# Performance work log

Measured on AMD Instinct MI355X. Metric: run time of the kernel, lower is better.

Reference implementation:

```python
import jax, jax.numpy as jnp
import numpy as np

B, V, E, H, L = 1024, 50257, 512, 512, 2


def setup_inputs() -> dict:
    key = jax.random.key(0)
    ks = jax.random.split(key, 12)
    s = 1.0 / np.sqrt(H)
    inp = {
        "x": jax.random.randint(ks[0], (B,), 0, V),
        "hidden": jnp.zeros((2 * L, B, H), jnp.float32),
        "embed": jax.random.normal(ks[1], (V, E), jnp.float32) * 0.02,
        # layer 0: input size E; layer 1: input size 2H (bidirectional concat)
        "Wih0": jax.random.uniform(ks[2], (2, 3 * H, E), jnp.float32, -s, s),
        "Whh0": jax.random.uniform(ks[3], (2, 3 * H, H), jnp.float32, -s, s),
        "bih0": jax.random.uniform(ks[4], (2, 3 * H), jnp.float32, -s, s),
        "bhh0": jax.random.uniform(ks[5], (2, 3 * H), jnp.float32, -s, s),
        "Wih1": jax.random.uniform(ks[6], (2, 3 * H, 2 * H), jnp.float32, -s, s),
        "Whh1": jax.random.uniform(ks[7], (2, 3 * H, H), jnp.float32, -s, s),
        "bih1": jax.random.uniform(ks[8], (2, 3 * H), jnp.float32, -s, s),
        "bhh1": jax.random.uniform(ks[9], (2, 3 * H), jnp.float32, -s, s),
        "Wproj": jax.random.uniform(ks[10], (V, E), jnp.float32, -1.0 / np.sqrt(E), 1.0 / np.sqrt(E)),
        "bproj": jax.random.uniform(ks[11], (V,), jnp.float32, -1.0 / np.sqrt(E), 1.0 / np.sqrt(E)),
    }
    return inp


def _gru_cell(x, h, Wih, Whh, bih, bhh):
    # PyTorch GRU cell: gates ordered (r, z, n)
    gi = x @ Wih.T + bih            # [B, 3H]
    gh = h @ Whh.T + bhh            # [B, 3H]
    ir, iz, inn = jnp.split(gi, 3, axis=-1)
    hr, hz, hn = jnp.split(gh, 3, axis=-1)
    r = jax.nn.sigmoid(ir + hr)
    z = jax.nn.sigmoid(iz + hz)
    n = jnp.tanh(inn + r * hn)
    return (1.0 - z) * n + z * h


def reference(x, hidden, embed, Wih0, Whh0, bih0, bhh0, Wih1, Whh1, bih1, bhh1, Wproj, bproj):
    inp = embed[x]                  # [B, E] embedding lookup; seq_len == 1
    layer_params = [(Wih0, Whh0, bih0, bhh0), (Wih1, Whh1, bih1, bhh1)]
    new_h = []
    for l, (Wih, Whh, bih, bhh) in enumerate(layer_params):
        # single timestep: fwd and bwd directions each do one cell step on the same input
        hf = _gru_cell(inp, hidden[2 * l],     Wih[0], Whh[0], bih[0], bhh[0])
        hb = _gru_cell(inp, hidden[2 * l + 1], Wih[1], Whh[1], bih[1], bhh[1])
        new_h += [hf, hb]
        inp = jnp.concatenate([hf, hb], axis=-1)   # [B, 2H]
    # x[:, :, hidden_dim:] -> backward-direction output of top layer, then transpose(0,1)
    out = hb[:, None, :]                            # [B, 1, H]
    logits = out @ Wproj.T + bproj                  # [B, 1, V]
    probs = jax.nn.softmax(logits, axis=-1)
    return probs, jnp.stack(new_h, axis=0)          # ([B,1,V], [2L, B, H])
```

## Files before the change

### kernel.cpp

```cpp
#include <hip/hip_runtime.h>


#define Bsz 1024
#define Hs  512
#define Vv  50257
#define VP2 50432
#define NG  1536
#define NPB2 197
#define NPBF 393

typedef __bf16 bf16x8 __attribute__((ext_vector_type(8)));
typedef float  floatx4 __attribute__((ext_vector_type(4)));

__device__ __forceinline__ unsigned short f2bf(float f) {
  unsigned int u = __builtin_bit_cast(unsigned int, f);
  u += 0x7fffu + ((u >> 16) & 1u);
  return (unsigned short)(u >> 16);
}

__device__ __forceinline__ float bf2f(unsigned short u) {
  unsigned int x = (unsigned int)u << 16;
  return __builtin_bit_cast(float, x);
}

__device__ __forceinline__ void cvt4(const float* src, unsigned short* dst) {
  float4 f = *(const float4*)src;
  unsigned int lo = (unsigned int)f2bf(f.x) | ((unsigned int)f2bf(f.y) << 16);
  unsigned int hi = (unsigned int)f2bf(f.z) | ((unsigned int)f2bf(f.w) << 16);
  *(uint2*)dst = make_uint2(lo, hi);
}

__device__ __forceinline__ void g2lds16(const void* g, void* l) {
  unsigned long long gv = (unsigned long long)g;
  unsigned int lv = (unsigned int)(unsigned long long)l;
  __builtin_amdgcn_global_load_lds(
      (const __attribute__((address_space(1))) unsigned int*)gv,
      (__attribute__((address_space(3))) unsigned int*)lv,
      16, 0, 0);
}

__device__ __forceinline__ void stage_half512(const unsigned short* src, long long rowBase,
                                              unsigned short* tile, int half, int kOff,
                                              int w, int l) {
#pragma unroll
  for (int i = 0; i < 2; ++i) {
    int t16 = (i * 8 + w) * 64 + l;
    int row = t16 >> 3, c = t16 & 7;
    int sc = c ^ (row & 7);
    const unsigned short* g = src + (rowBase + half * 128 + row) * 512ll + kOff + sc * 8;
    g2lds16(g, (char*)tile + half * 16384 + (i * 8 + w) * 1024 + l * 16);
  }
}

#define PHASEQ(Q)                                                                           \
  do {                                                                                      \
    bf16x8 afr[2][2];                                                                       \
    _Pragma("unroll") for (int mm = 0; mm < 2; ++mm)                                        \
    _Pragma("unroll") for (int ks = 0; ks < 2; ++ks) {                                      \
      int rowA = wr * 128 + (2 * (Q) + mm) * 16 + r16;                                      \
      int slot = (ks * 4 + g) ^ (rowA & 7);                                                 \
      afr[mm][ks] = *(const bf16x8*)((const char*)Ac + rowA * 128 + slot * 16);             \
    }                                                                                       \
    __builtin_amdgcn_s_barrier();                                                           \
    __builtin_amdgcn_s_setprio(1);                                                          \
    _Pragma("unroll") for (int ks = 0; ks < 2; ++ks)                                        \
    _Pragma("unroll") for (int mm = 0; mm < 2; ++mm)                                        \
    _Pragma("unroll") for (int nf = 0; nf < 4; ++nf)                                        \
      acc[2 * (Q) + mm][nf] = __builtin_amdgcn_mfma_f32_16x16x32_bf16(                      \
          afr[mm][ks], bfr[nf][ks], acc[2 * (Q) + mm][nf], 0, 0, 0);                        \
    __builtin_amdgcn_s_setprio(0);                                                          \
    __builtin_amdgcn_s_barrier();                                                           \
  } while (0)

__global__ __launch_bounds__(512, 2) void gemm_proj8(const unsigned short* A, const unsigned short* Bw,
                                                     const float* biasp, unsigned short* stash,
                                                     float* partial) {
  __shared__ alignas(16) unsigned short Ab[2][16384];
  __shared__ alignas(16) unsigned short Bb[2][16384];
  __shared__ float rowpart[256][4];
  const int tid = threadIdx.x;
  const int w = tid >> 6, l = tid & 63;
  const int wr = w >> 2, wc = w & 3;
  const int g = l >> 4, r16 = l & 15;
  int orig = blockIdx.x;
  int xcd = orig & 7, slot = orig >> 3;
  int wgid = (xcd < 4 ? xcd * 99 : 396 + (xcd - 4) * 98) + slot;
  int mt = wgid & 3, nt = wgid >> 2;

  floatx4 acc[8][4];
  floatx4 zero = {0.f, 0.f, 0.f, 0.f};
#pragma unroll
  for (int i = 0; i < 8; ++i)
#pragma unroll
    for (int j = 0; j < 4; ++j) acc[i][j] = zero;

  const long long mrb = (long long)mt * 256;
  const long long nrb = (long long)nt * 256;

  stage_half512(Bw, nrb, Bb[0], 0, 0, w, l);
  stage_half512(Bw, nrb, Bb[0], 1, 0, w, l);
  stage_half512(A,  mrb, Ab[0], 0, 0, w, l);
  stage_half512(A,  mrb, Ab[0], 1, 0, w, l);
  stage_half512(Bw, nrb, Bb[1], 0, 64, w, l);
  stage_half512(Bw, nrb, Bb[1], 1, 64, w, l);
  asm volatile("s_waitcnt vmcnt(4)" ::: "memory");
  __builtin_amdgcn_s_barrier();

#pragma unroll
  for (int t = 0; t < 8; ++t) {
    const int c = t & 1;
    const unsigned short* Ac = Ab[c];
    const unsigned short* Bc = Bb[c];
    if (t > 0) {
      if (t < 7) asm volatile("s_waitcnt vmcnt(4)" ::: "memory");
      else       asm volatile("s_waitcnt vmcnt(0)" ::: "memory");
      __builtin_amdgcn_s_barrier();
    }
    if (t + 1 < 8) stage_half512(A, mrb, Ab[c ^ 1], 0, (t + 1) * 64, w, l);
    bf16x8 bfr[4][2];
#pragma unroll
    for (int nf = 0; nf < 4; ++nf)
#pragma unroll
      for (int ks = 0; ks < 2; ++ks) {
        int rowB = wc * 64 + nf * 16 + r16;
        int slotb = (ks * 4 + g) ^ (rowB & 7);
        bfr[nf][ks] = *(const bf16x8*)((const char*)Bc + rowB * 128 + slotb * 16);
      }
    PHASEQ(0);
    if (t + 1 < 8) stage_half512(A, mrb, Ab[c ^ 1], 1, (t + 1) * 64, w, l);
    PHASEQ(1);
    if (t + 2 < 8) stage_half512(Bw, nrb, Bb[c], 0, (t + 2) * 64, w, l);
    PHASEQ(2);
    if (t + 2 < 8) stage_half512(Bw, nrb, Bb[c], 1, (t + 2) * 64, w, l);
    PHASEQ(3);
  }

  float bcol[4];
#pragma unroll
  for (int nf = 0; nf < 4; ++nf) bcol[nf] = biasp[nt * 256 + wc * 64 + nf * 16 + r16];
#pragma unroll
  for (int mf = 0; mf < 8; ++mf)
#pragma unroll
    for (int qq = 0; qq < 4; ++qq) {
      int rowl = wr * 128 + mf * 16 + g * 4 + qq;
      long long grow = mt * 256 + rowl;
      float s = 0.f;
#pragma unroll
      for (int nf = 0; nf < 4; ++nf) {
        int col = nt * 256 + wc * 64 + nf * 16 + r16;
        float v = __expf(acc[mf][nf][qq] + bcol[nf]);
        stash[grow * VP2 + col] = f2bf(v);
        s += v;
      }
      s += __shfl_xor(s, 1); s += __shfl_xor(s, 2);
      s += __shfl_xor(s, 4); s += __shfl_xor(s, 8);
      if (r16 == 0) rowpart[rowl][wc] = s;
    }
  __syncthreads();
  if (tid < 256) {
    float t4 = (rowpart[tid][0] + rowpart[tid][1]) + (rowpart[tid][2] + rowpart[tid][3]);
    partial[(size_t)(mt * 256 + tid) * NPB2 + nt] = t4;
  }
}

__device__ __forceinline__ void compute_step(const unsigned short* Acur, const unsigned short* Bcur,
                                             floatx4 (&acc)[4][4], int wr, int wc, int g, int r16) {
#pragma unroll
  for (int ks = 0; ks < 2; ++ks) {
    bf16x8 a[4], b[4];
#pragma unroll
    for (int i = 0; i < 4; ++i) {
      int rowA = wr * 64 + i * 16 + r16;
      int ca = (ks * 4 + g) ^ (rowA & 7);
      a[i] = *(const bf16x8*)((const char*)Acur + rowA * 128 + ca * 16);
      int rowB = wc * 64 + i * 16 + r16;
      int cb = (ks * 4 + g) ^ (rowB & 7);
      b[i] = *(const bf16x8*)((const char*)Bcur + rowB * 128 + cb * 16);
    }
#pragma unroll
    for (int i = 0; i < 4; ++i)
#pragma unroll
      for (int j = 0; j < 4; ++j)
        acc[i][j] = __builtin_amdgcn_mfma_f32_16x16x32_bf16(a[i], b[j], acc[i][j], 0, 0, 0);
  }
}

__device__ __forceinline__ void gemm_core8(const unsigned short* A, const unsigned short* Bw, int K,
                                           int mt, int nt,
                                           unsigned short* Alds, unsigned short* Blds,
                                           floatx4 (&acc)[4][4]) {
  const int tid = threadIdx.x;
  const int w = tid >> 6, l = tid & 63;
  const int wr = w >> 1, wc = w & 1;
  const int g = l >> 4, r16 = l & 15;
  floatx4 zero = {0.f, 0.f, 0.f, 0.f};
#pragma unroll
  for (int i = 0; i < 4; ++i)
#pragma unroll
    for (int j = 0; j < 4; ++j) acc[i][j] = zero;

  const int nsteps = K >> 6;
  for (int kt = 0; kt < nsteps; ++kt) {
    __syncthreads();
#pragma unroll
    for (int i = 0; i < 4; ++i) {
      int chunk = w * 4 + i;
      int t16 = chunk * 64 + l;
      int row = t16 >> 3, c = t16 & 7;
      int sc = c ^ (row & 7);
      g2lds16(A + (size_t)(mt * 256 + row) * K + kt * 64 + sc * 8, (char*)Alds + chunk * 1024);
    }
#pragma unroll
    for (int i = 0; i < 2; ++i) {
      int chunk = w * 2 + i;
      int t16 = chunk * 64 + l;
      int row = t16 >> 3, c = t16 & 7;
      int sc = c ^ (row & 7);
      g2lds16(Bw + (size_t)(nt * 128 + row) * K + kt * 64 + sc * 8, (char*)Blds + chunk * 1024);
    }
    __syncthreads();
    compute_step(Alds, Blds, acc, wr, wc, g, r16);
  }
}

struct GemmDesc {
  const unsigned short* A[4];
  const unsigned short* Bw[4];
  const float* bias[4];
  float* C[4];
  int K[4];
};

__global__ __launch_bounds__(512, 4) void gemm_gru_batch(GemmDesc d) {
  __shared__ alignas(16) unsigned short Alds[256 * 64];
  __shared__ alignas(16) unsigned short Blds[128 * 64];
  const int z = blockIdx.z;
  floatx4 acc[4][4];
  gemm_core8(d.A[z], d.Bw[z], d.K[z], blockIdx.y, blockIdx.x, Alds, Blds, acc);
  const float* bias = d.bias[z];
  float* C = d.C[z];
  const int tid = threadIdx.x, w = tid >> 6, l = tid & 63;
  const int wr = w >> 1, wc = w & 1, g = l >> 4, r16 = l & 15;
#pragma unroll
  for (int i = 0; i < 4; ++i)
#pragma unroll
    for (int j = 0; j < 4; ++j) {
      int col = blockIdx.x * 128 + wc * 64 + j * 16 + r16;
      float bc = bias[col];
#pragma unroll
      for (int q = 0; q < 4; ++q) {
        int row = blockIdx.y * 256 + wr * 64 + i * 16 + g * 4 + q;
        C[(size_t)row * NG + col] = acc[i][j][q] + bc;
      }
    }
}

__device__ __forceinline__ void gemm_coreBf32(const unsigned short* A, const float* Bw, int K,
                                              int mt, int nt, int maxrowB,
                                              unsigned short* Alds, unsigned short* Blds,
                                              floatx4 (&acc)[4][4]) {
  const int tid = threadIdx.x;
  const int w = tid >> 6, l = tid & 63;
  const int wr = w >> 1, wc = w & 1;
  const int g = l >> 4, r16 = l & 15;
  floatx4 zero = {0.f, 0.f, 0.f, 0.f};
#pragma unroll
  for (int i = 0; i < 4; ++i)
#pragma unroll
    for (int j = 0; j < 4; ++j) acc[i][j] = zero;
  int brow[2], bsc[2], brg[2];
#pragma unroll
  for (int i = 0; i < 2; ++i) {
    int chunk = w * 2 + i;
    int t16 = chunk * 64 + l;
    brow[i] = t16 >> 3;
    bsc[i] = (t16 & 7) ^ (brow[i] & 7);
    int rg = nt * 128 + brow[i];
    brg[i] = (rg > maxrowB) ? maxrowB : rg;
  }
  const int nsteps = K >> 6;
  for (int kt = 0; kt < nsteps; ++kt) {
    __syncthreads();
    float4 rb[2][2];
#pragma unroll
    for (int i = 0; i < 2; ++i) {
      const float* src = Bw + (size_t)brg[i] * K + kt * 64 + bsc[i] * 8;
      rb[i][0] = *(const float4*)src;
      rb[i][1] = *(const float4*)(src + 4);
    }
#pragma unroll
    for (int i = 0; i < 4; ++i) {
      int chunk = w * 4 + i;
      int t16 = chunk * 64 + l;
      int row = t16 >> 3, c = t16 & 7;
      int sc = c ^ (row & 7);
      g2lds16(A + (size_t)(mt * 256 + row) * K + kt * 64 + sc * 8, (char*)Alds + chunk * 1024);
    }
#pragma unroll
    for (int i = 0; i < 2; ++i) {
      uint4 p;
      p.x = (unsigned int)f2bf(rb[i][0].x) | ((unsigned int)f2bf(rb[i][0].y) << 16);
      p.y = (unsigned int)f2bf(rb[i][0].z) | ((unsigned int)f2bf(rb[i][0].w) << 16);
      p.z = (unsigned int)f2bf(rb[i][1].x) | ((unsigned int)f2bf(rb[i][1].y) << 16);
      p.w = (unsigned int)f2bf(rb[i][1].z) | ((unsigned int)f2bf(rb[i][1].w) << 16);
      *(uint4*)((char*)Blds + (w * 2 + i) * 1024 + l * 16) = p;
    }
    __syncthreads();
    compute_step(Alds, Blds, acc, wr, wc, g, r16);
  }
}

template <int MODE>
__global__ __launch_bounds__(512, 4) void gemm_proj_fb(const unsigned short* A, const float* Bw,
                                                       const float* biasp, float* probs,
                                                       float* partial, const float* inv) {
  __shared__ alignas(16) unsigned short Alds[256 * 64];
  __shared__ alignas(16) unsigned short Blds[128 * 64];
  __shared__ float rowpart[256];
  const int tid = threadIdx.x;
  if (MODE != 2 && tid < 256) rowpart[tid] = 0.f;
  int orig = blockIdx.x;
  int xcd = orig & 7, slot = orig >> 3;
  int wgid = (xcd < 4 ? xcd * 197 : 788 + (xcd - 4) * 196) + slot;
  int mt = wgid & 3, nt = wgid >> 2;
  floatx4 acc[4][4];
  gemm_coreBf32(A, Bw, 512, mt, nt, Vv - 1, Alds, Blds, acc);
  const int w = tid >> 6, l = tid & 63;
  const int wr = w >> 1, wc = w & 1, g = l >> 4, r16 = l & 15;
  float bcol[4];
#pragma unroll
  for (int j = 0; j < 4; ++j) bcol[j] = biasp[nt * 128 + wc * 64 + j * 16 + r16];
#pragma unroll
  for (int i = 0; i < 4; ++i)
#pragma unroll
    for (int q = 0; q < 4; ++q) {
      int rowl = wr * 64 + i * 16 + g * 4 + q;
      int grow = mt * 256 + rowl;
      float rinv = (MODE == 2) ? inv[grow] : 0.f;
      float s = 0.f;
#pragma unroll
      for (int j = 0; j < 4; ++j) {
        int col = nt * 128 + wc * 64 + j * 16 + r16;
        float v = __expf(acc[i][j][q] + bcol[j]);
        if (MODE == 2) { if (col < Vv) probs[(size_t)grow * Vv + col] = v * rinv; }
        s += v;
      }
      if (MODE != 2) {
        s += __shfl_xor(s, 1); s += __shfl_xor(s, 2);
        s += __shfl_xor(s, 4); s += __shfl_xor(s, 8);
        if (r16 == 0) atomicAdd(&rowpart[rowl], s);
      }
    }
  if (MODE != 2) {
    __syncthreads();
    if (tid < 256) partial[(size_t)(mt * 256 + tid) * NPBF + nt] = rowpart[tid];
  }
}

__global__ __launch_bounds__(256) void gru_gates(const float* Cbuf, const float* hidden,
                                                 float* out_newh, unsigned short* bf_out, int layer) {
  int idx = blockIdx.x * 256 + threadIdx.x;
  int j = idx & 511;
  int b = (idx >> 9) & 1023;
  int d = idx >> 19;
  const float* GI = Cbuf + (size_t)d * Bsz * NG;
  const float* GH = Cbuf + (size_t)(2 + d) * Bsz * NG;
  size_t base = (size_t)b * NG + j;
  float ir = GI[base], iz = GI[base + 512], inn = GI[base + 1024];
  float hr = GH[base], hz = GH[base + 512], hn = GH[base + 1024];
  float r = 1.f / (1.f + __expf(-(ir + hr)));
  float z = 1.f / (1.f + __expf(-(iz + hz)));
  float n = tanhf(inn + r * hn);
  size_t hoff = (size_t)(2 * layer + d) * (Bsz * Hs) + (size_t)b * Hs + j;
  float hprev = hidden[hoff];
  float h = (1.f - z) * n + z * hprev;
  out_newh[hoff] = h;
  if (layer == 0) {
    bf_out[(size_t)b * 1024 + d * 512 + j] = f2bf(h);
  } else if (d == 1) {
    bf_out[(size_t)b * 512 + j] = f2bf(h);
  }
}

__global__ void convert_all(const float* Wih0, const float* Whh0, const float* Wih1, const float* Whh1,
                            const float* hidden, const float* Wproj, const float* bproj,
                            unsigned short* wih0b, unsigned short* whh0b, unsigned short* wih1b,
                            unsigned short* whh1b, unsigned short* hbf, unsigned short* wprojb,
                            float* bprojp) {
  long long idx = ((long long)blockIdx.x * 256 + threadIdx.x) * 4;
  if (idx < 1572864) { cvt4(Wih0 + idx, wih0b + idx); return; }
  idx -= 1572864;
  if (idx < 1572864) { cvt4(Whh0 + idx, whh0b + idx); return; }
  idx -= 1572864;
  if (idx < 3145728) { cvt4(Wih1 + idx, wih1b + idx); return; }
  idx -= 3145728;
  if (idx < 1572864) { cvt4(Whh1 + idx, whh1b + idx); return; }
  idx -= 1572864;
  if (idx < 2097152) { cvt4(hidden + idx, hbf + idx); return; }
  idx -= 2097152;
  if (idx < 25821184) {
    long long row = idx >> 9, col = idx & 511;
    if (row < Vv) cvt4(Wproj + row * 512 + col, wprojb + idx);
    else *(uint2*)(wprojb + idx) = make_uint2(0u, 0u);
    return;
  }
  idx -= 25821184;
  if (idx < VP2) {
    float4 v;
    v.x = (idx + 0 < Vv) ? bproj[idx + 0] : -1e30f;
    v.y = (idx + 1 < Vv) ? bproj[idx + 1] : -1e30f;
    v.z = (idx + 2 < Vv) ? bproj[idx + 2] : -1e30f;
    v.w = (idx + 3 < Vv) ? bproj[idx + 3] : -1e30f;
    *(float4*)(bprojp + idx) = v;
  }
}

__global__ void gather_embed(const int* x, const float* embed, unsigned short* xe) {
  int b = blockIdx.x, t = threadIdx.x;
  int tok = x[b];
  float2 v = *(const float2*)(embed + (size_t)tok * 512 + t * 2);
  unsigned int o = ((unsigned int)f2bf(v.y) << 16) | f2bf(v.x);
  *(unsigned int*)((unsigned short*)xe + (size_t)b * 512 + t * 2) = o;
}

__global__ void rowsum_inv(const float* partial, float* inv, int npb) {
  int row = blockIdx.x, tid = threadIdx.x;
  float s = 0.f;
  for (int c = tid; c < npb; c += 128) s += partial[(size_t)row * npb + c];
  __shared__ float tmp[128];
  tmp[tid] = s;
  __syncthreads();
  for (int off = 64; off > 0; off >>= 1) {
    if (tid < off) tmp[tid] += tmp[tid + off];
    __syncthreads();
  }
  if (tid == 0) inv[row] = 1.0f / tmp[0];
}

__global__ __launch_bounds__(256) void scale_expand(const unsigned short* stash, const float* inv,
                                                    float* probs) {
  const unsigned int nquad = 12865792u;
  const unsigned int step = gridDim.x * 256u;
  for (unsigned int f = blockIdx.x * 256u + threadIdx.x; f < nquad; f += step) {
    unsigned int e0 = f * 4u;
    unsigned int row = e0 / (unsigned int)Vv;
    int col = (int)(e0 - row * (unsigned int)Vv);
    float4 o;
    if (col + 4 <= Vv) {
      float s = inv[row];
      const unsigned short* sp = stash + (size_t)row * VP2 + col;
      if ((col & 1) == 0) {
        unsigned int u0 = *(const unsigned int*)sp;
        unsigned int u1 = *(const unsigned int*)(sp + 2);
        o.x = bf2f((unsigned short)u0) * s;
        o.y = bf2f((unsigned short)(u0 >> 16)) * s;
        o.z = bf2f((unsigned short)u1) * s;
        o.w = bf2f((unsigned short)(u1 >> 16)) * s;
      } else {
        o.x = bf2f(sp[0]) * s; o.y = bf2f(sp[1]) * s;
        o.z = bf2f(sp[2]) * s; o.w = bf2f(sp[3]) * s;
      }
    } else {
      float vals[4];
#pragma unroll
      for (int k = 0; k < 4; ++k) {
        unsigned int e = e0 + k;
        unsigned int rk = e / (unsigned int)Vv;
        int ck = (int)(e - rk * (unsigned int)Vv);
        vals[k] = bf2f(stash[(size_t)rk * VP2 + ck]) * inv[rk];
      }
      o.x = vals[0]; o.y = vals[1]; o.z = vals[2]; o.w = vals[3];
    }
    *(float4*)(probs + e0) = o;
  }
}

extern "C" void kernel_launch(void* const* d_in, const int* in_sizes, int n_in,
                              void* d_out, int out_size, void* d_ws, size_t ws_size,
                              hipStream_t stream) {
  const int*   x      = (const int*)d_in[0];
  const float* hidden = (const float*)d_in[1];
  const float* embed  = (const float*)d_in[2];
  const float* Wih0   = (const float*)d_in[3];
  const float* Whh0   = (const float*)d_in[4];
  const float* bih0   = (const float*)d_in[5];
  const float* bhh0   = (const float*)d_in[6];
  const float* Wih1   = (const float*)d_in[7];
  const float* Whh1   = (const float*)d_in[8];
  const float* bih1   = (const float*)d_in[9];
  const float* bhh1   = (const float*)d_in[10];
  const float* Wproj  = (const float*)d_in[11];
  const float* bproj  = (const float*)d_in[12];
  float* out = (float*)d_out;

  char* ws = (char*)d_ws;
  unsigned short* wih0b  = (unsigned short*)(ws);
  unsigned short* whh0b  = (unsigned short*)(ws + 3145728);
  unsigned short* wih1b  = (unsigned short*)(ws + 6291456);
  unsigned short* whh1b  = (unsigned short*)(ws + 12582912);
  unsigned short* hbf    = (unsigned short*)(ws + 15728640);
  float*          bprojp = (float*)(ws + 19922944);
  unsigned short* xe     = (unsigned short*)(ws + 20124672);
  unsigned short* inp1   = (unsigned short*)(ws + 21173248);
  unsigned short* hb1    = (unsigned short*)(ws + 23270400);
  unsigned short* wprojb = (unsigned short*)(ws + 24318976);
  float*          partial= (float*)(ws + 75961344);
  float*          inv    = (float*)(ws + 77571072);
  float*          Cbuf   = (float*)(ws + 77575168);
  unsigned short* stash  = (unsigned short*)(ws + 77575168);
  const size_t NEED_STASH = 77575168ull + (size_t)Bsz * VP2 * 2ull;

  float* out_newh = out + 51463168ll;

  convert_all<<<34994, 256, 0, stream>>>(Wih0, Whh0, Wih1, Whh1, hidden, Wproj, bproj,
                                         wih0b, whh0b, wih1b, whh1b, hbf, wprojb, bprojp);
  gather_embed<<<1024, 256, 0, stream>>>(x, embed, xe);

  GemmDesc d0;
  d0.A[0] = xe;  d0.A[1] = xe;
  d0.A[2] = hbf; d0.A[3] = hbf + 524288;
  d0.Bw[0] = wih0b; d0.Bw[1] = wih0b + 786432;
  d0.Bw[2] = whh0b; d0.Bw[3] = whh0b + 786432;
  d0.bias[0] = bih0; d0.bias[1] = bih0 + 1536;
  d0.bias[2] = bhh0; d0.bias[3] = bhh0 + 1536;
  d0.C[0] = Cbuf;             d0.C[1] = Cbuf + 1572864;
  d0.C[2] = Cbuf + 2*1572864; d0.C[3] = Cbuf + 3*1572864;
  d0.K[0] = d0.K[1] = d0.K[2] = d0.K[3] = 512;
  gemm_gru_batch<<<dim3(12, 4, 4), 512, 0, stream>>>(d0);
  gru_gates<<<4096, 256, 0, stream>>>(Cbuf, hidden, out_newh, inp1, 0);

  GemmDesc d1;
  d1.A[0] = inp1; d1.A[1] = inp1;
  d1.A[2] = hbf + 2*524288; d1.A[3] = hbf + 3*524288;
  d1.Bw[0] = wih1b; d1.Bw[1] = wih1b + 1572864;
  d1.Bw[2] = whh1b; d1.Bw[3] = whh1b + 786432;
  d1.bias[0] = bih1; d1.bias[1] = bih1 + 1536;
  d1.bias[2] = bhh1; d1.bias[3] = bhh1 + 1536;
  d1.C[0] = Cbuf;             d1.C[1] = Cbuf + 1572864;
  d1.C[2] = Cbuf + 2*1572864; d1.C[3] = Cbuf + 3*1572864;
  d1.K[0] = d1.K[1] = 1024; d1.K[2] = d1.K[3] = 512;
  gemm_gru_batch<<<dim3(12, 4, 4), 512, 0, stream>>>(d1);
  gru_gates<<<4096, 256, 0, stream>>>(Cbuf, hidden, out_newh, hb1, 1);

  if (ws_size >= NEED_STASH) {
    gemm_proj8<<<788, 512, 0, stream>>>(hb1, wprojb, bprojp, stash, partial);
    rowsum_inv<<<1024, 128, 0, stream>>>(partial, inv, NPB2);
    scale_expand<<<8192, 256, 0, stream>>>(stash, inv, out);
  } else {
    gemm_proj_fb<1><<<1572, 512, 0, stream>>>(hb1, Wproj, bprojp, out, partial, inv);
    rowsum_inv<<<1024, 128, 0, stream>>>(partial, inv, NPBF);
    gemm_proj_fb<2><<<1572, 512, 0, stream>>>(hb1, Wproj, bprojp, out, partial, inv);
  }
}
```

Measured before the change: 251.1 us.

## Overlap Wproj bf16 conversion with GRU GEMMs and coalesce projection stash stores

The large Wproj fp32-to-bf16 conversion leaves the upfront convert kernel. It is split into two halves, each run by an extra z-slice of blocks inside the two GRU GEMM launches, so it overlaps with those small, latency-bound GEMMs. The GRU GEMM tile shrinks from 256x128 with 512 threads to 128x128 with 256 threads, which doubles the block count. The projection GEMM epilogue now writes exp values into a swizzled LDS pool and then copies them to the stash with 16-byte coalesced stores, replacing scattered 2-byte writes. This adds an extra barrier and LDS traffic, and conversion blocks compete with the GEMM blocks for bandwidth and CUs.

Measured after the change: 371.6 us. +48.0%, slower.

```diff
diff --git a/kernel.cpp b/kernel.cpp
--- a/kernel.cpp
+++ b/kernel.cpp
@@ -75,9 +75,10 @@
 __global__ __launch_bounds__(512, 2) void gemm_proj8(const unsigned short* A, const unsigned short* Bw,
                                                      const float* biasp, unsigned short* stash,
                                                      float* partial) {
-  __shared__ alignas(16) unsigned short Ab[2][16384];
-  __shared__ alignas(16) unsigned short Bb[2][16384];
+  __shared__ alignas(16) unsigned short POOL[65536];
   __shared__ float rowpart[256][4];
+  unsigned short* Ab[2] = { POOL, POOL + 16384 };
+  unsigned short* Bb[2] = { POOL + 32768, POOL + 49152 };
   const int tid = threadIdx.x;
   const int w = tid >> 6, l = tid & 63;
   const int wr = w >> 2, wc = w & 3;
@@ -135,6 +136,7 @@
     PHASEQ(3);
   }
 
+  __syncthreads();
   float bcol[4];
 #pragma unroll
   for (int nf = 0; nf < 4; ++nf) bcol[nf] = biasp[nt * 256 + wc * 64 + nf * 16 + r16];
@@ -143,13 +145,13 @@
 #pragma unroll
     for (int qq = 0; qq < 4; ++qq) {
       int rowl = wr * 128 + mf * 16 + g * 4 + qq;
-      long long grow = mt * 256 + rowl;
+      int swz = ((rowl >> 2) & 3) << 4;
       float s = 0.f;
 #pragma unroll
       for (int nf = 0; nf < 4; ++nf) {
-        int col = nt * 256 + wc * 64 + nf * 16 + r16;
+        int col = wc * 64 + nf * 16 + r16;
         float v = __expf(acc[mf][nf][qq] + bcol[nf]);
-        stash[grow * VP2 + col] = f2bf(v);
+        POOL[(rowl * 256 + col) ^ swz] = f2bf(v);
         s += v;
       }
       s += __shfl_xor(s, 1); s += __shfl_xor(s, 2);
@@ -159,7 +161,15 @@
   __syncthreads();
   if (tid < 256) {
     float t4 = (rowpart[tid][0] + rowpart[tid][1]) + (rowpart[tid][2] + rowpart[tid][3]);
-    partial[(size_t)(mt * 256 + tid) * NPB2 + nt] = t4;
+    partial[(size_t)(mt * 256 + tid) * NPB2 + tid * 0 + nt] = t4;
+  }
+#pragma unroll
+  for (int p = 0; p < 16; ++p) {
+    int r = p * 16 + (tid >> 5);
+    int c16 = tid & 31;
+    int idx = (r * 256 + c16 * 8) ^ (((r >> 2) & 3) << 4);
+    uint4 v = *(const uint4*)(POOL + idx);
+    *(uint4*)(stash + (size_t)(mt * 256 + r) * VP2 + nt * 256 + c16 * 8) = v;
   }
 }
 
@@ -185,10 +195,10 @@
   }
 }
 
-__device__ __forceinline__ void gemm_core8(const unsigned short* A, const unsigned short* Bw, int K,
-                                           int mt, int nt,
-                                           unsigned short* Alds, unsigned short* Blds,
-                                           floatx4 (&acc)[4][4]) {
+__device__ __forceinline__ void gemm_core128(const unsigned short* A, const unsigned short* Bw, int K,
+                                             int mt, int nt,
+                                             unsigned short* Alds, unsigned short* Blds,
+                                             floatx4 (&acc)[4][4]) {
   const int tid = threadIdx.x;
   const int w = tid >> 6, l = tid & 63;
   const int wr = w >> 1, wc = w & 1;
@@ -208,11 +218,11 @@
       int t16 = chunk * 64 + l;
       int row = t16 >> 3, c = t16 & 7;
       int sc = c ^ (row & 7);
-      g2lds16(A + (size_t)(mt * 256 + row) * K + kt * 64 + sc * 8, (char*)Alds + chunk * 1024);
-    }
-#pragma unroll
-    for (int i = 0; i < 2; ++i) {
-      int chunk = w * 2 + i;
+      g2lds16(A + (size_t)(mt * 128 + row) * K + kt * 64 + sc * 8, (char*)Alds + chunk * 1024);
+    }
+#pragma unroll
+    for (int i = 0; i < 4; ++i) {
+      int chunk = w * 4 + i;
       int t16 = chunk * 64 + l;
       int row = t16 >> 3, c = t16 & 7;
       int sc = c ^ (row & 7);
@@ -231,12 +241,26 @@
   int K[4];
 };
 
-__global__ __launch_bounds__(512, 4) void gemm_gru_batch(GemmDesc d) {
-  __shared__ alignas(16) unsigned short Alds[256 * 64];
+__global__ __launch_bounds__(256, 4) void gemm_gru_batch(GemmDesc d, const float* Wproj,
+                                                         unsigned short* wprojb, int convPhase) {
+  if (blockIdx.z == 4) {
+    const long long HALF = 3227648;
+    long long b = (long long)blockIdx.y * 12 + blockIdx.x;
+    long long start = b * 33622;
+    long long end = start + 33622; if (end > HALF) end = HALF;
+    for (long long u = start + threadIdx.x; u < end; u += 256) {
+      long long idx = ((long long)convPhase * HALF + u) * 4;
+      long long row = idx >> 9, colk = idx & 511;
+      if (row < Vv) cvt4(Wproj + row * 512 + colk, wprojb + idx);
+      else *(uint2*)(wprojb + idx) = make_uint2(0u, 0u);
+    }
+    return;
+  }
+  __shared__ alignas(16) unsigned short Alds[128 * 64];
   __shared__ alignas(16) unsigned short Blds[128 * 64];
   const int z = blockIdx.z;
   floatx4 acc[4][4];
-  gemm_core8(d.A[z], d.Bw[z], d.K[z], blockIdx.y, blockIdx.x, Alds, Blds, acc);
+  gemm_core128(d.A[z], d.Bw[z], d.K[z], blockIdx.y, blockIdx.x, Alds, Blds, acc);
   const float* bias = d.bias[z];
   float* C = d.C[z];
   const int tid = threadIdx.x, w = tid >> 6, l = tid & 63;
@@ -249,10 +273,15 @@
       float bc = bias[col];
 #pragma unroll
       for (int q = 0; q < 4; ++q) {
-        int row = blockIdx.y * 256 + wr * 64 + i * 16 + g * 4 + q;
+        int row = blockIdx.y * 128 + wr * 64 + i * 16 + g * 4 + q;
         C[(size_t)row * NG + col] = acc[i][j][q] + bc;
       }
     }
+}
+
+__device__ __forceinline__ void compute_step8(const unsigned short* Acur, const unsigned short* Bcur,
+                                              floatx4 (&acc)[4][4], int wr, int wc, int g, int r16) {
+  compute_step(Acur, Bcur, acc, wr, wc, g, r16);
 }
 
 __device__ __forceinline__ void gemm_coreBf32(const unsigned short* A, const float* Bw, int K,
@@ -306,7 +335,7 @@
       *(uint4*)((char*)Blds + (w * 2 + i) * 1024 + l * 16) = p;
     }
     __syncthreads();
-    compute_step(Alds, Blds, acc, wr, wc, g, r16);
+    compute_step8(Alds, Blds, acc, wr, wc, g, r16);
   }
 }
 
@@ -382,11 +411,10 @@
   }
 }
 
-__global__ void convert_all(const float* Wih0, const float* Whh0, const float* Wih1, const float* Whh1,
-                            const float* hidden, const float* Wproj, const float* bproj,
-                            unsigned short* wih0b, unsigned short* whh0b, unsigned short* wih1b,
-                            unsigned short* whh1b, unsigned short* hbf, unsigned short* wprojb,
-                            float* bprojp) {
+__global__ void convert_small(const float* Wih0, const float* Whh0, const float* Wih1,
+                              const float* Whh1, const float* hidden, const float* bproj,
+                              unsigned short* wih0b, unsigned short* whh0b, unsigned short* wih1b,
+                              unsigned short* whh1b, unsigned short* hbf, float* bprojp) {
   long long idx = ((long long)blockIdx.x * 256 + threadIdx.x) * 4;
   if (idx < 1572864) { cvt4(Wih0 + idx, wih0b + idx); return; }
   idx -= 1572864;
@@ -398,13 +426,6 @@
   idx -= 1572864;
   if (idx < 2097152) { cvt4(hidden + idx, hbf + idx); return; }
   idx -= 2097152;
-  if (idx < 25821184) {
-    long long row = idx >> 9, col = idx & 511;
-    if (row < Vv) cvt4(Wproj + row * 512 + col, wprojb + idx);
-    else *(uint2*)(wprojb + idx) = make_uint2(0u, 0u);
-    return;
-  }
-  idx -= 25821184;
   if (idx < VP2) {
     float4 v;
     v.x = (idx + 0 < Vv) ? bproj[idx + 0] : -1e30f;
@@ -512,9 +533,11 @@
 
   float* out_newh = out + 51463168ll;
 
-  convert_all<<<34994, 256, 0, stream>>>(Wih0, Whh0, Wih1, Whh1, hidden, Wproj, bproj,
-                                         wih0b, whh0b, wih1b, whh1b, hbf, wprojb, bprojp);
+  convert_small<<<9778, 256, 0, stream>>>(Wih0, Whh0, Wih1, Whh1, hidden, bproj,
+                                          wih0b, whh0b, wih1b, whh1b, hbf, bprojp);
   gather_embed<<<1024, 256, 0, stream>>>(x, embed, xe);
+
+  const bool stash_path = (ws_size >= NEED_STASH);
 
   GemmDesc d0;
   d0.A[0] = xe;  d0.A[1] = xe;
@@ -526,7 +549,7 @@
   d0.C[0] = Cbuf;             d0.C[1] = Cbuf + 1572864;
   d0.C[2] = Cbuf + 2*1572864; d0.C[3] = Cbuf + 3*1572864;
   d0.K[0] = d0.K[1] = d0.K[2] = d0.K[3] = 512;
-  gemm_gru_batch<<<dim3(12, 4, 4), 512, 0, stream>>>(d0);
+  gemm_gru_batch<<<dim3(12, 8, stash_path ? 5 : 4), 256, 0, stream>>>(d0, Wproj, wprojb, 0);
   gru_gates<<<4096, 256, 0, stream>>>(Cbuf, hidden, out_newh, inp1, 0);
 
   GemmDesc d1;
@@ -539,10 +562,10 @@
   d1.C[0] = Cbuf;             d1.C[1] = Cbuf + 1572864;
   d1.C[2] = Cbuf + 2*1572864; d1.C[3] = Cbuf + 3*1572864;
   d1.K[0] = d1.K[1] = 1024; d1.K[2] = d1.K[3] = 512;
-  gemm_gru_batch<<<dim3(12, 4, 4), 512, 0, stream>>>(d1);
+  gemm_gru_batch<<<dim3(12, 8, stash_path ? 5 : 4), 256, 0, stream>>>(d1, Wproj, wprojb, 1);
   gru_gates<<<4096, 256, 0, stream>>>(Cbuf, hidden, out_newh, hb1, 1);
 
-  if (ws_size >= NEED_STASH) {
+  if (stash_path) {
     gemm_proj8<<<788, 512, 0, stream>>>(hb1, wprojb, bprojp, stash, partial);
     rowsum_inv<<<1024, 128, 0, stream>>>(partial, inv, NPB2);
     scale_expand<<<8192, 256, 0, stream>>>(stash, inv, out);
```
